# Performance work log

Measured on AMD Instinct MI355X. Metric: run time of the kernel, lower is better.

## Reference

```python
import jax, jax.numpy as jnp
import numpy as np

S, B, I, H, L = 512, 64, 1024, 1024, 2


def setup_inputs() -> dict:
    key = jax.random.key(0)
    ks = jax.random.split(key, 1 + 4 * L)
    inp = {"x": jax.random.normal(ks[0], (S, B, I), dtype=jnp.float32)}
    scale = 1.0 / np.sqrt(H)
    for l in range(L):
        in_size = I if l == 0 else H
        k0, k1, k2, k3 = ks[1 + 4 * l: 5 + 4 * l]
        inp[f"Wih{l}"] = jax.random.normal(k0, (in_size, 4 * H), dtype=jnp.float32) * scale
        inp[f"bih{l}"] = jax.random.normal(k1, (4 * H,), dtype=jnp.float32) * scale
        inp[f"Whh{l}"] = jax.random.normal(k2, (H, 4 * H), dtype=jnp.float32) * scale
        inp[f"bhh{l}"] = jax.random.normal(k3, (4 * H,), dtype=jnp.float32) * scale
    return inp


def _lstm_forward(x, Wih, bih, Whh, bhh):
    # x: [S,B,I]; Wih[l]: [in,4H]; Whh[l]: [H,4H]
    batch = x.shape[1]
    h0 = tuple(jnp.zeros((batch, H), x.dtype) for _ in range(L))
    c0 = tuple(jnp.zeros((batch, H), x.dtype) for _ in range(L))

    def step(carry, x_t):
        hs, cs = carry
        new_hs, new_cs = [], []
        inp = x_t
        for l in range(L):
            gates = inp @ Wih[l] + bih[l] + hs[l] @ Whh[l] + bhh[l]  # [B,4H]
            i_g, f_g, o_g, g_g = jnp.split(gates, 4, axis=1)
            c = jax.nn.sigmoid(f_g) * cs[l] + jax.nn.sigmoid(i_g) * jnp.tanh(g_g)
            h = jax.nn.sigmoid(o_g) * jnp.tanh(c)
            new_hs.append(h)
            new_cs.append(c)
            inp = h
        return (tuple(new_hs), tuple(new_cs)), inp

    (hs, cs), output = jax.lax.scan(step, (h0, c0), x)
    return output, jnp.stack(hs), jnp.stack(cs)


def reference(x, Wih0, bih0, Whh0, bhh0, Wih1, bih1, Whh1, bhh1):
    Wih = [Wih0, Wih1]
    bih = [bih0, bih1]
    Whh = [Whh0, Whh1]
    bhh = [bhh0, bhh1]
    output, h_n, c_n = _lstm_forward(x, Wih, bih, Whh, bhh)
    return output, h_n, c_n
```

## Files before the change

kernel.cpp:

```cpp
#include <hip/hip_runtime.h>


typedef unsigned short bhalf;
typedef __attribute__((ext_vector_type(8))) short s8v;
typedef __attribute__((ext_vector_type(4))) float f32x4;
typedef __attribute__((ext_vector_type(2))) unsigned int u32x2;

__device__ __forceinline__ float bf2f(bhalf u) {
    unsigned int x = ((unsigned int)u) << 16;
    return __builtin_bit_cast(float, x);
}
__device__ __forceinline__ bhalf f2bf(float f) {
    unsigned int x = __builtin_bit_cast(unsigned int, f);
    unsigned int r = (x + 0x7fffu + ((x >> 16) & 1u)) >> 16;
    return (bhalf)r;
}
__device__ __forceinline__ float sigf(float x) { return 1.f / (1.f + __expf(-x)); }
__device__ __forceinline__ float tanh_(float x) { return 2.f / (1.f + __expf(-2.f * x)) - 1.f; }

__device__ __forceinline__ void pollge(const int* p, int target) {
    if (target <= 0) return;
    int it = 0;
    while (__hip_atomic_load(p, __ATOMIC_RELAXED, __HIP_MEMORY_SCOPE_AGENT) < target) {
        __builtin_amdgcn_s_sleep(1);
        if (++it > 50000000) break;
    }
}

__global__ __launch_bounds__(256) void init_k(
    const float* __restrict__ bih0, const float* __restrict__ bhh0,
    const float* __restrict__ bih1, const float* __restrict__ bhh1,
    float* bias0, float* bias1, bhalf* h0z, bhalf* h1z,
    float* c0, float* c1, int* flags)
{
    int i = blockIdx.x * 256 + threadIdx.x;
    h0z[i] = 0; h1z[i] = 0; c0[i] = 0.f; c1[i] = 0.f;
    if (i < 6144) flags[i] = 0;
    if (i < 4096) {
        bias0[i] = bih0[i] + bhh0[i];
        bias1[i] = bih1[i] + bhh1[i];
    }
}

__global__ __launch_bounds__(256) void transpose_k(
    const float* __restrict__ src, bhalf* __restrict__ dst, int dstStride, int kOff)
{
    __shared__ float T[64][65];
    int kb = blockIdx.x & 15;
    int nb = blockIdx.x >> 4;
    int k0 = kb << 6, n0 = nb << 6;
    int tid = threadIdx.x;
    #pragma unroll
    for (int i = 0; i < 16; ++i) {
        int lin = (i << 8) + tid;
        int r = lin >> 6, c = lin & 63;
        T[r][c] = src[(size_t)(k0 + r) * 4096 + n0 + c];
    }
    __syncthreads();
    #pragma unroll
    for (int i = 0; i < 16; ++i) {
        int lin = (i << 8) + tid;
        int r = lin >> 6, c = lin & 63;
        dst[(size_t)(n0 + r) * dstStride + kOff + k0 + c] = f2bf(T[c][r]);
    }
}

__global__ __launch_bounds__(256) void g0gemm_k(
    const float* __restrict__ x, const bhalf* __restrict__ WT,
    const float* __restrict__ bias0, bhalf* __restrict__ G0,
    int t0, int bmCount)
{
    __shared__ __align__(16) bhalf Xs[128 * 72];
    __shared__ __align__(16) bhalf Ws[128 * 72];
    const int tid = threadIdx.x;
    const int bm = blockIdx.x % bmCount;
    const int bn = blockIdx.x / bmCount;
    const int row0 = bm << 7;
    const int n0 = bn << 7;
    const int wid = tid >> 6, lane = tid & 63;
    const int wm = wid >> 1, wn = wid & 1;
    const int row16 = lane & 15, koff = (lane >> 4) << 3;

    f32x4 acc[4][4];
    const f32x4 zero4 = {0.f, 0.f, 0.f, 0.f};
    #pragma unroll
    for (int mt = 0; mt < 4; ++mt)
        #pragma unroll
        for (int nt = 0; nt < 4; ++nt) acc[mt][nt] = zero4;

    const float* xbase = x + (size_t)(t0 * 64 + row0) * 1024;
    for (int kc = 0; kc < 16; ++kc) {
        __syncthreads();
        #pragma unroll
        for (int j = 0; j < 8; ++j) {
            int e = (((j << 8) + tid) << 2);
            int r = e >> 6, k = e & 63;
            f32x4 xv = *(const f32x4*)(xbase + (size_t)r * 1024 + (kc << 6) + k);
            u32x2 p;
            p.x = (unsigned)f2bf(xv.x) | ((unsigned)f2bf(xv.y) << 16);
            p.y = (unsigned)f2bf(xv.z) | ((unsigned)f2bf(xv.w) << 16);
            *(u32x2*)&Xs[r * 72 + k] = p;
        }
        #pragma unroll
        for (int j = 0; j < 4; ++j) {
            int e = (((j << 8) + tid) << 3);
            int r = e >> 6, k = e & 63;
            *(s8v*)&Ws[r * 72 + k] = *(const s8v*)(WT + (size_t)(n0 + r) * 1024 + (kc << 6) + k);
        }
        __syncthreads();
        #pragma unroll
        for (int ks = 0; ks < 2; ++ks) {
            int kk = ks << 5;
            s8v a[4], b[4];
            #pragma unroll
            for (int mt = 0; mt < 4; ++mt)
                a[mt] = *(const s8v*)&Xs[(wm * 64 + mt * 16 + row16) * 72 + kk + koff];
            #pragma unroll
            for (int nt = 0; nt < 4; ++nt)
                b[nt] = *(const s8v*)&Ws[(wn * 64 + nt * 16 + row16) * 72 + kk + koff];
            #pragma unroll
            for (int mt = 0; mt < 4; ++mt)
                #pragma unroll
                for (int nt = 0; nt < 4; ++nt)
                    acc[mt][nt] = __builtin_amdgcn_mfma_f32_16x16x32_bf16(a[mt], b[nt], acc[mt][nt], 0, 0, 0);
        }
    }
    #pragma unroll
    for (int mt = 0; mt < 4; ++mt)
        #pragma unroll
        for (int nt = 0; nt < 4; ++nt) {
            int gcol = n0 + wn * 64 + nt * 16 + row16;
            float bz = bias0[gcol];
            #pragma unroll
            for (int r = 0; r < 4; ++r) {
                int grow = row0 + wm * 64 + mt * 16 + ((lane >> 4) << 2) + r;
                G0[((size_t)grow << 12) + gcol] = f2bf(acc[mt][nt][r] + bz);
            }
        }
}

template <bool IS_L0>
__device__ __forceinline__ void rec_loop(
    const bhalf* Wlds, float* gatesLds,
    const bhalf* __restrict__ G0, const float* __restrict__ bias1,
    bhalf* h0buf, bhalf* h1buf, float* cws,
    int* done0, int* done1, float* out,
    int t0, int nsteps, int smask, int wgIdx)
{
    constexpr int NMT = IS_L0 ? 4 : 2;
    constexpr int NH  = IS_L0 ? 16 : 8;
    const int tid = threadIdx.x;
    const int wid = tid >> 6, lane = tid & 63;
    const int row16 = lane & 15;
    const int koff = (lane >> 4) << 3;
    const int hcBase = wgIdx * NH;
    const f32x4 zero4 = {0.f, 0.f, 0.f, 0.f};

    const bool ep_active = IS_L0 ? true : (tid < 128);
    const int eb  = IS_L0 ? (tid >> 2) : (tid >> 1);
    const int ejq = (IS_L0 ? (tid & 3) : (tid & 1)) << 2;
    const int ehc = hcBase + ejq;

    float creg[4] = {0.f, 0.f, 0.f, 0.f};
    float breg[4][4];
    if (ep_active) {
        #pragma unroll
        for (int j = 0; j < 4; ++j) creg[j] = cws[(eb << 10) + ehc + j];
        if (!IS_L0)
            #pragma unroll
            for (int g = 0; g < 4; ++g)
                #pragma unroll
                for (int j = 0; j < 4; ++j) breg[g][j] = bias1[(g << 10) + ehc + j];
    }
    int* myflag = IS_L0 ? &done0[wgIdx * 32] : &done1[wgIdx * 32];

    for (int tl = 0; tl < nsteps; ++tl) {
        const int t = t0 + tl;

        u32x2 g0pre[4];
        if (IS_L0) {
            const bhalf* gp = G0 + (((size_t)tl * 64 + eb) << 12) + ehc;
            #pragma unroll
            for (int g = 0; g < 4; ++g) g0pre[g] = *(const u32x2*)(gp + (g << 10));
        }

        if (IS_L0) {
            if (wid == 0)      pollge(&done0[lane * 32], t);
        } else {
            if (wid == 0)      pollge(&done0[lane * 32], t + 1);
            else if (wid == 1) pollge(&done1[lane * 32], t);
            else if (wid == 2) pollge(&done1[(64 + lane) * 32], t);
        }
        __syncthreads();

        const int prev = (tl - 1) & smask;
        const bhalf* h0r = h0buf + ((size_t)prev << 16);
        const bhalf* h0c = h0buf + ((size_t)tl << 16);
        const bhalf* h1r = h1buf + ((size_t)prev << 16);
        const int brow = (wid << 4) + row16;

        f32x4 acc[NMT];
        #pragma unroll
        for (int mt = 0; mt < NMT; ++mt) acc[mt] = zero4;

        if (IS_L0) {
            s8v bfr[32];
            #pragma unroll
            for (int ks = 0; ks < 32; ++ks)
                bfr[ks] = *(const s8v*)(h0r + brow * 1024 + (ks << 5) + koff);
            #pragma unroll
            for (int ks = 0; ks < 32; ++ks)
                #pragma unroll
                for (int mt = 0; mt < 4; ++mt) {
                    s8v a = *(const s8v*)&Wlds[((((mt << 5) + ks) << 6) + lane) << 3];
                    acc[mt] = __builtin_amdgcn_mfma_f32_16x16x32_bf16(a, bfr[ks], acc[mt], 0, 0, 0);
                }
        } else {
            s8v bfa[32], bfb[32];
            #pragma unroll
            for (int ks = 0; ks < 32; ++ks)
                bfa[ks] = *(const s8v*)(h0c + brow * 1024 + (ks << 5) + koff);
            #pragma unroll
            for (int ks = 0; ks < 32; ++ks)
                bfb[ks] = *(const s8v*)(h1r + brow * 1024 + (ks << 5) + koff);
            #pragma unroll
            for (int ks = 0; ks < 32; ++ks)
                #pragma unroll
                for (int mt = 0; mt < 2; ++mt) {
                    s8v a = *(const s8v*)&Wlds[((((mt << 6) + ks) << 6) + lane) << 3];
                    acc[mt] = __builtin_amdgcn_mfma_f32_16x16x32_bf16(a, bfa[ks], acc[mt], 0, 0, 0);
                }
            #pragma unroll
            for (int ks = 0; ks < 32; ++ks)
                #pragma unroll
                for (int mt = 0; mt < 2; ++mt) {
                    s8v a = *(const s8v*)&Wlds[((((mt << 6) + 32 + ks) << 6) + lane) << 3];
                    acc[mt] = __builtin_amdgcn_mfma_f32_16x16x32_bf16(a, bfb[ks], acc[mt], 0, 0, 0);
                }
        }
        #pragma unroll
        for (int mt = 0; mt < NMT; ++mt)
            #pragma unroll
            for (int r = 0; r < 4; ++r) {
                int ci = (mt << 4) + ((lane >> 4) << 2) + r;
                gatesLds[ci * 68 + brow] = acc[mt][r];
            }
        __syncthreads();

        float hv[4] = {0.f, 0.f, 0.f, 0.f};
        if (ep_active) {
            float ga[4][4];
            #pragma unroll
            for (int g = 0; g < 4; ++g)
                #pragma unroll
                for (int j = 0; j < 4; ++j)
                    ga[g][j] = gatesLds[(g * NH + ejq + j) * 68 + eb];
            if (IS_L0) {
                #pragma unroll
                for (int g = 0; g < 4; ++g) {
                    ga[g][0] += bf2f((bhalf)(g0pre[g].x & 0xffffu));
                    ga[g][1] += bf2f((bhalf)(g0pre[g].x >> 16));
                    ga[g][2] += bf2f((bhalf)(g0pre[g].y & 0xffffu));
                    ga[g][3] += bf2f((bhalf)(g0pre[g].y >> 16));
                }
            } else {
                #pragma unroll
                for (int g = 0; g < 4; ++g)
                    #pragma unroll
                    for (int j = 0; j < 4; ++j) ga[g][j] += breg[g][j];
            }
            #pragma unroll
            for (int j = 0; j < 4; ++j) {
                float cn = sigf(ga[1][j]) * creg[j] + sigf(ga[0][j]) * tanh_(ga[3][j]);
                creg[j] = cn;
                hv[j] = sigf(ga[2][j]) * tanh_(cn);
            }
            u32x2 hp;
            hp.x = (unsigned)f2bf(hv[0]) | ((unsigned)f2bf(hv[1]) << 16);
            hp.y = (unsigned)f2bf(hv[2]) | ((unsigned)f2bf(hv[3]) << 16);
            unsigned long long hpu = __builtin_bit_cast(unsigned long long, hp);
            const int ix = (eb << 10) + ehc;
            bhalf* hdst = (IS_L0 ? h0buf : h1buf) + ((size_t)tl << 16) + ix;
            __hip_atomic_store((unsigned long long*)hdst, hpu,
                               __ATOMIC_RELAXED, __HIP_MEMORY_SCOPE_AGENT);
        }
        asm volatile("s_waitcnt vmcnt(0)" ::: "memory");
        __syncthreads();
        if (tid == 0)
            __hip_atomic_store(myflag, t + 1, __ATOMIC_RELAXED, __HIP_MEMORY_SCOPE_AGENT);
        if (!IS_L0 && ep_active) {
            f32x4 ov = {hv[0], hv[1], hv[2], hv[3]};
            *(f32x4*)(out + (((size_t)t * 64 + eb) << 10) + ehc) = ov;
        }
    }

    if (ep_active) {
        #pragma unroll
        for (int j = 0; j < 4; ++j) cws[(eb << 10) + ehc + j] = creg[j];
    }
}

__global__ __launch_bounds__(256, 1) void rec_k(
    const bhalf* __restrict__ W0T, const bhalf* __restrict__ W1T,
    const bhalf* __restrict__ G0, const float* __restrict__ bias1,
    bhalf* h0buf, bhalf* h1buf, float* c0ws, float* c1ws,
    int* done0, int* done1, float* out, int t0, int nsteps, int smask)
{
    __shared__ __align__(16) bhalf Wlds[65536];
    __shared__ __align__(16) float gatesLds[64 * 68];
    const int tid = threadIdx.x;
    const int wg = blockIdx.x;
    if (wg < 64) {
        for (int it = 0; it < 32; ++it) {
            int e = (((it << 8) + tid) << 3);
            int ci = e >> 10, k0 = e & 1023;
            int n = ((ci >> 4) << 10) + (wg << 4) + (ci & 15);
            int mt = ci >> 4, m = ci & 15, ks = k0 >> 5, q = (k0 >> 3) & 3;
            int off = ((((mt << 5) + ks) << 6) + (q << 4) + m) << 3;
            *(s8v*)&Wlds[off] = *(const s8v*)(W0T + ((size_t)n << 10) + k0);
        }
        __syncthreads();
        rec_loop<true>(Wlds, gatesLds, G0, bias1, h0buf, h1buf, c0ws,
                       done0, done1, out, t0, nsteps, smask, wg);
    } else {
        int wg1 = wg - 64;
        for (int it = 0; it < 32; ++it) {
            int e = (((it << 8) + tid) << 3);
            int ci = e >> 11, k0 = e & 2047;
            int n = ((ci >> 3) << 10) + (wg1 << 3) + (ci & 7);
            int mt = ci >> 4, m = ci & 15, ks = k0 >> 5, q = (k0 >> 3) & 3;
            int off = ((((mt << 6) + ks) << 6) + (q << 4) + m) << 3;
            *(s8v*)&Wlds[off] = *(const s8v*)(W1T + ((size_t)n << 11) + k0);
        }
        __syncthreads();
        rec_loop<false>(Wlds, gatesLds, G0, bias1, h0buf, h1buf, c1ws,
                        done0, done1, out, t0, nsteps, smask, wg1);
    }
}

__global__ __launch_bounds__(256) void tail_k(
    const bhalf* __restrict__ h0f, const bhalf* __restrict__ h1f,
    const float* __restrict__ c0, const float* __restrict__ c1, float* dst)
{
    int i = blockIdx.x * 256 + threadIdx.x;
    if (i >= 131072) return;
    int l = i >> 16, r = i & 65535;
    dst[i] = bf2f(l ? h1f[r] : h0f[r]);
    dst[131072 + i] = l ? c1[r] : c0[r];
}

extern "C" void kernel_launch(void* const* d_in, const int* in_sizes, int n_in,
                              void* d_out, int out_size, void* d_ws, size_t ws_size,
                              hipStream_t stream) {
    const float* x    = (const float*)d_in[0];
    const float* Wih0 = (const float*)d_in[1];
    const float* bih0 = (const float*)d_in[2];
    const float* Whh0 = (const float*)d_in[3];
    const float* bhh0 = (const float*)d_in[4];
    const float* Wih1 = (const float*)d_in[5];
    const float* bih1 = (const float*)d_in[6];
    const float* Whh1 = (const float*)d_in[7];
    const float* bhh1 = (const float*)d_in[8];
    float* out = (float*)d_out;
    char* ws = (char*)d_ws;

    bhalf* WT0ih = (bhalf*)(ws);
    bhalf* WT0hh = (bhalf*)(ws + 8388608);
    bhalf* WT1   = (bhalf*)(ws + 16777216);
    float* bias0 = (float*)(ws + 33554432);
    float* bias1 = (float*)(ws + 33570816);
    float* c0    = (float*)(ws + 33587200);
    float* c1    = (float*)(ws + 33849344);
    int*   done0 = (int*)(ws + 34111488);
    int*   done1 = (int*)(ws + 34119680);
    const size_t fixedSz = 34136064;

    int CHUNK = 8;
    for (int c = 512; c >= 8; c >>= 1)
        if (fixedSz + (size_t)c * (131072 + 131072 + 524288) <= ws_size) { CHUNK = c; break; }

    bhalf* h0buf = (bhalf*)(ws + fixedSz);
    bhalf* h1buf = (bhalf*)(ws + fixedSz + (size_t)CHUNK * 131072);
    bhalf* G0    = (bhalf*)(ws + fixedSz + (size_t)CHUNK * 262144);

    init_k<<<256, 256, 0, stream>>>(bih0, bhh0, bih1, bhh1, bias0, bias1,
                                    h0buf + (size_t)(CHUNK - 1) * 65536,
                                    h1buf + (size_t)(CHUNK - 1) * 65536,
                                    c0, c1, done0);
    transpose_k<<<1024, 256, 0, stream>>>(Wih0, WT0ih, 1024, 0);
    transpose_k<<<1024, 256, 0, stream>>>(Whh0, WT0hh, 1024, 0);
    transpose_k<<<1024, 256, 0, stream>>>(Wih1, WT1, 2048, 0);
    transpose_k<<<1024, 256, 0, stream>>>(Whh1, WT1, 2048, 1024);

    for (int t0 = 0; t0 < 512; t0 += CHUNK) {
        int bmCount = CHUNK / 2;
        g0gemm_k<<<bmCount * 32, 256, 0, stream>>>(x, WT0ih, bias0, G0, t0, bmCount);
        rec_k<<<192, 256, 0, stream>>>(WT0hh, WT1, G0, bias1, h0buf, h1buf,
                                       c0, c1, done0, done1, out, t0, CHUNK, CHUNK - 1);
    }
    tail_k<<<512, 256, 0, stream>>>(h0buf + (size_t)(CHUNK - 1) * 65536,
                                    h1buf + (size_t)(CHUNK - 1) * 65536,
                                    c0, c1, out + 33554432);
}
```

Measured before the change: 7.573 ms.

## Compute LSTM cell epilogue directly from MFMA accumulators, dropping LDS gate transpose

Reorders the weight rows loaded into LDS so that each lane's MFMA accumulator already holds all four gates (i, f, o, g) for its own hidden units. The cell update then runs straight from registers, removing the gate scatter to shared memory, one __syncthreads, and the idle half of threads in the layer-1 epilogue. This cuts per-step latency on the serial recurrent critical path. In exchange, h stores and output writes become narrower (2 elements per lane in layer 1) and the mapping of weight rows is more intricate.

Result: faster. 7.333 ms (-3.2%).

```diff
diff --git a/kernel.cpp b/kernel.cpp
--- a/kernel.cpp
+++ b/kernel.cpp
@@ -4,6 +4,7 @@
 typedef unsigned short bhalf;
 typedef __attribute__((ext_vector_type(8))) short s8v;
 typedef __attribute__((ext_vector_type(4))) float f32x4;
+typedef __attribute__((ext_vector_type(2))) float f32x2;
 typedef __attribute__((ext_vector_type(2))) unsigned int u32x2;
 
 __device__ __forceinline__ float bf2f(bhalf u) {
@@ -17,6 +18,10 @@
 }
 __device__ __forceinline__ float sigf(float x) { return 1.f / (1.f + __expf(-x)); }
 __device__ __forceinline__ float tanh_(float x) { return 2.f / (1.f + __expf(-2.f * x)) - 1.f; }
+__device__ __forceinline__ float g0elem(u32x2 p, int r) {
+    unsigned u = (r & 2) ? p.y : p.x;
+    return bf2f((bhalf)((r & 1) ? (u >> 16) : (u & 0xffffu)));
+}
 
 __device__ __forceinline__ void pollge(const int* p, int target) {
     if (target <= 0) return;
@@ -141,36 +146,37 @@
 
 template <bool IS_L0>
 __device__ __forceinline__ void rec_loop(
-    const bhalf* Wlds, float* gatesLds,
+    const bhalf* Wlds,
     const bhalf* __restrict__ G0, const float* __restrict__ bias1,
     bhalf* h0buf, bhalf* h1buf, float* cws,
     int* done0, int* done1, float* out,
     int t0, int nsteps, int smask, int wgIdx)
 {
     constexpr int NMT = IS_L0 ? 4 : 2;
-    constexpr int NH  = IS_L0 ? 16 : 8;
+    constexpr int NC  = IS_L0 ? 4 : 2;
     const int tid = threadIdx.x;
     const int wid = tid >> 6, lane = tid & 63;
     const int row16 = lane & 15;
-    const int koff = (lane >> 4) << 3;
-    const int hcBase = wgIdx * NH;
+    const int q = lane >> 4;
+    const int koff = q << 3;
+    const int batch = (wid << 4) + row16;
+    const int myhc = IS_L0 ? ((wgIdx << 4) + (q << 2))
+                           : ((wgIdx << 3) + (q << 1));
     const f32x4 zero4 = {0.f, 0.f, 0.f, 0.f};
 
-    const bool ep_active = IS_L0 ? true : (tid < 128);
-    const int eb  = IS_L0 ? (tid >> 2) : (tid >> 1);
-    const int ejq = (IS_L0 ? (tid & 3) : (tid & 1)) << 2;
-    const int ehc = hcBase + ejq;
-
-    float creg[4] = {0.f, 0.f, 0.f, 0.f};
-    float breg[4][4];
-    if (ep_active) {
-        #pragma unroll
-        for (int j = 0; j < 4; ++j) creg[j] = cws[(eb << 10) + ehc + j];
-        if (!IS_L0)
-            #pragma unroll
-            for (int g = 0; g < 4; ++g)
-                #pragma unroll
-                for (int j = 0; j < 4; ++j) breg[g][j] = bias1[(g << 10) + ehc + j];
+    float creg[NC];
+    {
+        const float* cp = cws + ((size_t)batch << 10) + myhc;
+        #pragma unroll
+        for (int j = 0; j < NC; ++j) creg[j] = cp[j];
+    }
+    float breg[4][2];
+    if (!IS_L0) {
+        #pragma unroll
+        for (int g = 0; g < 4; ++g) {
+            f32x2 b2 = *(const f32x2*)(bias1 + (g << 10) + myhc);
+            breg[g][0] = b2.x; breg[g][1] = b2.y;
+        }
     }
     int* myflag = IS_L0 ? &done0[wgIdx * 32] : &done1[wgIdx * 32];
 
@@ -179,13 +185,13 @@
 
         u32x2 g0pre[4];
         if (IS_L0) {
-            const bhalf* gp = G0 + (((size_t)tl * 64 + eb) << 12) + ehc;
+            const bhalf* gp = G0 + (((size_t)tl * 64 + batch) << 12) + myhc;
             #pragma unroll
             for (int g = 0; g < 4; ++g) g0pre[g] = *(const u32x2*)(gp + (g << 10));
         }
 
         if (IS_L0) {
-            if (wid == 0)      pollge(&done0[lane * 32], t);
+            if (wid == 0) pollge(&done0[lane * 32], t);
         } else {
             if (wid == 0)      pollge(&done0[lane * 32], t + 1);
             else if (wid == 1) pollge(&done1[lane * 32], t);
@@ -197,7 +203,6 @@
         const bhalf* h0r = h0buf + ((size_t)prev << 16);
         const bhalf* h0c = h0buf + ((size_t)tl << 16);
         const bhalf* h1r = h1buf + ((size_t)prev << 16);
-        const int brow = (wid << 4) + row16;
 
         f32x4 acc[NMT];
         #pragma unroll
@@ -207,7 +212,7 @@
             s8v bfr[32];
             #pragma unroll
             for (int ks = 0; ks < 32; ++ks)
-                bfr[ks] = *(const s8v*)(h0r + brow * 1024 + (ks << 5) + koff);
+                bfr[ks] = *(const s8v*)(h0r + batch * 1024 + (ks << 5) + koff);
             #pragma unroll
             for (int ks = 0; ks < 32; ++ks)
                 #pragma unroll
@@ -219,10 +224,10 @@
             s8v bfa[32], bfb[32];
             #pragma unroll
             for (int ks = 0; ks < 32; ++ks)
-                bfa[ks] = *(const s8v*)(h0c + brow * 1024 + (ks << 5) + koff);
-            #pragma unroll
-            for (int ks = 0; ks < 32; ++ks)
-                bfb[ks] = *(const s8v*)(h1r + brow * 1024 + (ks << 5) + koff);
+                bfa[ks] = *(const s8v*)(h0c + batch * 1024 + (ks << 5) + koff);
+            #pragma unroll
+            for (int ks = 0; ks < 32; ++ks)
+                bfb[ks] = *(const s8v*)(h1r + batch * 1024 + (ks << 5) + koff);
             #pragma unroll
             for (int ks = 0; ks < 32; ++ks)
                 #pragma unroll
@@ -238,65 +243,58 @@
                     acc[mt] = __builtin_amdgcn_mfma_f32_16x16x32_bf16(a, bfb[ks], acc[mt], 0, 0, 0);
                 }
         }
-        #pragma unroll
-        for (int mt = 0; mt < NMT; ++mt)
+
+        float hvo[2];
+        if (IS_L0) {
+            float hv[4];
             #pragma unroll
             for (int r = 0; r < 4; ++r) {
-                int ci = (mt << 4) + ((lane >> 4) << 2) + r;
-                gatesLds[ci * 68 + brow] = acc[mt][r];
-            }
-        __syncthreads();
-
-        float hv[4] = {0.f, 0.f, 0.f, 0.f};
-        if (ep_active) {
-            float ga[4][4];
-            #pragma unroll
-            for (int g = 0; g < 4; ++g)
-                #pragma unroll
-                for (int j = 0; j < 4; ++j)
-                    ga[g][j] = gatesLds[(g * NH + ejq + j) * 68 + eb];
-            if (IS_L0) {
-                #pragma unroll
-                for (int g = 0; g < 4; ++g) {
-                    ga[g][0] += bf2f((bhalf)(g0pre[g].x & 0xffffu));
-                    ga[g][1] += bf2f((bhalf)(g0pre[g].x >> 16));
-                    ga[g][2] += bf2f((bhalf)(g0pre[g].y & 0xffffu));
-                    ga[g][3] += bf2f((bhalf)(g0pre[g].y >> 16));
-                }
-            } else {
-                #pragma unroll
-                for (int g = 0; g < 4; ++g)
-                    #pragma unroll
-                    for (int j = 0; j < 4; ++j) ga[g][j] += breg[g][j];
-            }
-            #pragma unroll
-            for (int j = 0; j < 4; ++j) {
-                float cn = sigf(ga[1][j]) * creg[j] + sigf(ga[0][j]) * tanh_(ga[3][j]);
-                creg[j] = cn;
-                hv[j] = sigf(ga[2][j]) * tanh_(cn);
+                float gi = acc[0][r] + g0elem(g0pre[0], r);
+                float gf = acc[1][r] + g0elem(g0pre[1], r);
+                float go = acc[2][r] + g0elem(g0pre[2], r);
+                float gg = acc[3][r] + g0elem(g0pre[3], r);
+                float cn = sigf(gf) * creg[r] + sigf(gi) * tanh_(gg);
+                creg[r] = cn;
+                hv[r] = sigf(go) * tanh_(cn);
             }
             u32x2 hp;
             hp.x = (unsigned)f2bf(hv[0]) | ((unsigned)f2bf(hv[1]) << 16);
             hp.y = (unsigned)f2bf(hv[2]) | ((unsigned)f2bf(hv[3]) << 16);
             unsigned long long hpu = __builtin_bit_cast(unsigned long long, hp);
-            const int ix = (eb << 10) + ehc;
-            bhalf* hdst = (IS_L0 ? h0buf : h1buf) + ((size_t)tl << 16) + ix;
+            bhalf* hdst = h0buf + ((size_t)tl << 16) + (batch << 10) + myhc;
             __hip_atomic_store((unsigned long long*)hdst, hpu,
                                __ATOMIC_RELAXED, __HIP_MEMORY_SCOPE_AGENT);
-        }
+        } else {
+            #pragma unroll
+            for (int j = 0; j < 2; ++j) {
+                float gi = acc[0][2 * j]     + breg[0][j];
+                float gf = acc[1][2 * j]     + breg[1][j];
+                float go = acc[0][2 * j + 1] + breg[2][j];
+                float gg = acc[1][2 * j + 1] + breg[3][j];
+                float cn = sigf(gf) * creg[j] + sigf(gi) * tanh_(gg);
+                creg[j] = cn;
+                hvo[j] = sigf(go) * tanh_(cn);
+            }
+            unsigned hp = (unsigned)f2bf(hvo[0]) | ((unsigned)f2bf(hvo[1]) << 16);
+            bhalf* hdst = h1buf + ((size_t)tl << 16) + (batch << 10) + myhc;
+            __hip_atomic_store((unsigned*)hdst, hp,
+                               __ATOMIC_RELAXED, __HIP_MEMORY_SCOPE_AGENT);
+        }
+
         asm volatile("s_waitcnt vmcnt(0)" ::: "memory");
         __syncthreads();
         if (tid == 0)
             __hip_atomic_store(myflag, t + 1, __ATOMIC_RELAXED, __HIP_MEMORY_SCOPE_AGENT);
-        if (!IS_L0 && ep_active) {
-            f32x4 ov = {hv[0], hv[1], hv[2], hv[3]};
-            *(f32x4*)(out + (((size_t)t * 64 + eb) << 10) + ehc) = ov;
-        }
-    }
-
-    if (ep_active) {
-        #pragma unroll
-        for (int j = 0; j < 4; ++j) cws[(eb << 10) + ehc + j] = creg[j];
+        if (!IS_L0) {
+            f32x2 ov = {hvo[0], hvo[1]};
+            *(f32x2*)(out + (((size_t)t * 64 + batch) << 10) + myhc) = ov;
+        }
+    }
+
+    {
+        float* cp = cws + ((size_t)batch << 10) + myhc;
+        #pragma unroll
+        for (int j = 0; j < NC; ++j) cp[j] = creg[j];
     }
 }
 
@@ -307,7 +305,6 @@
     int* done0, int* done1, float* out, int t0, int nsteps, int smask)
 {
     __shared__ __align__(16) bhalf Wlds[65536];
-    __shared__ __align__(16) float gatesLds[64 * 68];
     const int tid = threadIdx.x;
     const int wg = blockIdx.x;
     if (wg < 64) {
@@ -315,25 +312,26 @@
             int e = (((it << 8) + tid) << 3);
             int ci = e >> 10, k0 = e & 1023;
             int n = ((ci >> 4) << 10) + (wg << 4) + (ci & 15);
-            int mt = ci >> 4, m = ci & 15, ks = k0 >> 5, q = (k0 >> 3) & 3;
-            int off = ((((mt << 5) + ks) << 6) + (q << 4) + m) << 3;
+            int mt = ci >> 4, m = ci & 15, ks = k0 >> 5, qk = (k0 >> 3) & 3;
+            int off = ((((mt << 5) + ks) << 6) + (qk << 4) + m) << 3;
             *(s8v*)&Wlds[off] = *(const s8v*)(W0T + ((size_t)n << 10) + k0);
         }
         __syncthreads();
-        rec_loop<true>(Wlds, gatesLds, G0, bias1, h0buf, h1buf, c0ws,
+        rec_loop<true>(Wlds, G0, bias1, h0buf, h1buf, c0ws,
                        done0, done1, out, t0, nsteps, smask, wg);
     } else {
         int wg1 = wg - 64;
         for (int it = 0; it < 32; ++it) {
             int e = (((it << 8) + tid) << 3);
             int ci = e >> 11, k0 = e & 2047;
-            int n = ((ci >> 3) << 10) + (wg1 << 3) + (ci & 7);
-            int mt = ci >> 4, m = ci & 15, ks = k0 >> 5, q = (k0 >> 3) & 3;
-            int off = ((((mt << 6) + ks) << 6) + (q << 4) + m) << 3;
+            int g  = (ci >> 4) + ((ci & 1) << 1);
+            int n  = (g << 10) + (wg1 << 3) + ((ci >> 1) & 7);
+            int mt = ci >> 4, m = ci & 15, ks = k0 >> 5, qk = (k0 >> 3) & 3;
+            int off = ((((mt << 6) + ks) << 6) + (qk << 4) + m) << 3;
             *(s8v*)&Wlds[off] = *(const s8v*)(W1T + ((size_t)n << 11) + k0);
         }
         __syncthreads();
-        rec_loop<false>(Wlds, gatesLds, G0, bias1, h0buf, h1buf, c1ws,
+        rec_loop<false>(Wlds, G0, bias1, h0buf, h1buf, c1ws,
                         done0, done1, out, t0, nsteps, smask, wg1);
     }
 }
```
